# Optimization experiments

Measured on AMD Instinct MI355X. Metric: run time of the kernel, lower is better.

The kernel has to match this reference:

```python
import jax, jax.numpy as jnp
import numpy as np

CAL = {
 'x': (-0.0025095, 0.0022181),
 'onnxMatMul_166': (-0.22075387835502625, 0.208940327167511),
 'fc1MatMul': (-0.00291599917, 0.0017367251),
 'fc1bias': (-0.48688140511512756, 0.5176185369491577),
 'fc1Add': (-0.48778465390205383, 0.5181604027748108),
 'Wiz_1': (-0.43284985423088074, 0.46175122261047363),
 'Wir_1': (-0.34401071071624756, 0.29191476106643677),
 'Win_1': (-0.3236880302429199, 0.39607325196266174),
 'Whz_1': (-1.8417714834213257, 1.7173254489898682),
 'Whr_1': (-1.1574513912200928, 1.0300449132919312),
 'Whn_1': (-0.7756922245025635, 0.9530389308929443),
 'biz_1': (-0.5063393712043762, 0.36664387583732605),
 'bir_1': (-0.07920225709676743, 0.20611026883125305),
 'bin_1': (-0.5539973378181458, 0.17938342690467834),
 'bhz_1': (-0.5337516665458679, 0.4148772358894348),
 'bhr_1': (-0.07688436657190323, 0.14814253151416779),
 'bhn_1': (-0.7828555107116699, 0.9008108973503113),
 'Wiz_2': (-0.9102030992507935, 0.9408696889877319),
 'Wir_2': (-0.9560997486114502, 0.6683358550071716),
 'Win_2': (-0.4721935987472534, 0.48561596870422363),
 'Whz_2': (-1.2992678880691528, 1.2991048097610474),
 'Whr_2': (-0.8318714499473572, 1.1085889339447021),
 'Whn_2': (-0.955470085144043, 1.046797513961792),
 'biz_2': (-0.44805487990379333, 0.1560053527355194),
 'bir_2': (-0.08767592161893845, 0.11347303539514542),
 'bin_2': (-0.239909827709198, 0.12033259868621826),
 'bhz_2': (-0.43745461106300354, 0.12699371576309204),
 'bhr_2': (-0.09617264568805695, 0.07690174877643585),
 'bhn_2': (-0.17204178869724274, 0.19739042222499847),
 'onnxMatMul_207': (-1.3657219409942627, 1.158295750617981),
 'fc2bias': (-0.1750922054052353, 0.1385071724653244),
 'onnxMatMul_208': (-3.1666038036346436, 2.5026357173919678),
 'fc3bias': (-0.10188056528568268, 0.0899151861667633),
 'onnxMatMul_209': (-1.300571084022522, 1.928941249847412),
 'fc4bias': (-0.10699586570262909, 0.04597663879394531),
 'h1': (-0.002647488145157695, 0.0028339680284261703),
 'h2': (-0.0031016061548143625, 0.0030250486452132463),
 'gru1_a_': (-0.6389939785003662, 0.7715625762939453),
 'gru1_a': (-0.6046768426895142, 0.8871182203292847),
 'gru1_b_': (-0.004922409541904926, 0.004103424027562141),
 'gru1_b': (-0.07475128024816513, 0.14630259573459625),
 'gru1_c_': (-1.5660111904144287, 1.0454494953155518),
 'gru1_c': (-1.9779117107391357, 1.3700535297393799),
 'gru1_d_': (-0.008429044857621193, 0.006403823848813772),
 'gru1_d': (-0.5529640316963196, 0.41507571935653687),
 'gru1_e_': (-1.3637111186981201, 1.018247127532959),
 'gru1_e': (-1.8583884239196777, 1.1587692499160767),
 'gru1_f_': (-0.005411399528384209, 0.0061536869034171104),
 'gru1_f': (-0.7833794355392456, 0.8978855013847351),
 'gru1_r_': (-0.6226556301116943, 0.9800534844398499),
 'gru1_r': (0.3491777181625366, 0.7271188497543335),
 'gru1_z_': (-2.392332077026367, 1.7851293087005615),
 'gru1_z': (0.08375928550958633, 0.856329083442688),
 'gru1_n1': (-0.5516456365585327, 0.4556601643562317),
 'gru1_n2': (-2.4100341796875, 1.1423156261444092),
 'gru1_n': (-0.983996570110321, 0.8151924014091492),
 'gru1_hn1': (0.143670916557312, 0.9162406921386719),
 'gru1_hn2': (-0.9015777111053467, 0.45391541719436646),
 'gru1_hn3': (-0.0016954239690676332, 0.0016671211924403906),
 'rnn1GRU': (-0.9016271829605103, 0.4546271562576294),
 'gru2_a_': (-0.681461751461029, 0.9113116264343262),
 'gru2_a': (-0.7149235010147095, 0.908741295337677),
 'gru2_b_': (-0.005148397758603096, 0.011014967225492),
 'gru2_b': (-0.09436552226543427, 0.07623167335987091),
 'gru2_c_': (-1.2279887199401855, 1.1102137565612793),
 'gru2_c': (-1.6760436296463013, 1.200895071029663),
 'gru2_d_': (-0.008141756057739258, 0.00894666276872158),
 'gru2_d': (-0.43875735998153687, 0.1262134611606598),
 'gru2_e_': (-0.6732944250106812, 0.6314664483070374),
}
# calib entries for gru2 past 'e_' were truncated in the source; reuse gru1 ranges
for _k in ['e', 'f_', 'f', 'r_', 'r', 'z_', 'z', 'n1', 'n2', 'n', 'hn1', 'hn2', 'hn3']:
    CAL.setdefault('gru2_' + _k, CAL['gru1_' + _k])
CAL['rnn2GRU'] = CAL['rnn1GRU']


def fq(x, name):
    """Per-tensor unsigned 8-bit fake-quantize/dequantize (CalibrationParam S/Z)."""
    mn, mx = CAL[name]
    s = (mx - mn) / 255.0  # 2**8 - 1
    z = float(round(-mn / s))
    q = jnp.clip(jnp.round(x / s) + z, 0.0, 255.0)
    y = (q - z) * s
    # straight-through: forward value is exact fake-quant, identity gradient
    return x + jax.lax.stop_gradient(y - x)


def _gru_layer(xs, Wiz, Wir, Win, Whz, Whr, Whn, biz, bir, binn, bhz, bhr, bhn, L):
    p = 'gru%d' % L
    Wiz = fq(Wiz, 'Wiz_%d' % L); Wir = fq(Wir, 'Wir_%d' % L); Win = fq(Win, 'Win_%d' % L)
    Whz = fq(Whz, 'Whz_%d' % L); Whr = fq(Whr, 'Whr_%d' % L); Whn = fq(Whn, 'Whn_%d' % L)
    biz = fq(biz, 'biz_%d' % L); bir = fq(bir, 'bir_%d' % L); binn = fq(binn, 'bin_%d' % L)
    bhz = fq(bhz, 'bhz_%d' % L); bhr = fq(bhr, 'bhr_%d' % L); bhn = fq(bhn, 'bhn_%d' % L)
    # input projections batched over all timesteps (xs: [T,B,H] time-major)
    A = fq(fq(jnp.einsum('tbi,ih->tbh', xs, Wir), p + '_a_') + bir, p + '_a')
    C = fq(fq(jnp.einsum('tbi,ih->tbh', xs, Wiz), p + '_c_') + biz, p + '_c')
    E = fq(fq(jnp.einsum('tbi,ih->tbh', xs, Win), p + '_e_') + binn, p + '_e')
    h0 = fq(jnp.zeros((xs.shape[1], Whz.shape[0]), xs.dtype), 'h%d' % L)

    def step(h, ace):
        a, c, e = ace
        b = fq(fq(h @ Whr, p + '_b_') + bhr, p + '_b')
        r = fq(jax.nn.sigmoid(fq(a + b, p + '_r_')), p + '_r')
        d = fq(fq(h @ Whz, p + '_d_') + bhz, p + '_d')
        z = fq(jax.nn.sigmoid(fq(c + d, p + '_z_')), p + '_z')
        f = fq(fq(h @ Whn, p + '_f_') + bhn, p + '_f')
        n = fq(jnp.tanh(fq(e + fq(r * f, p + '_n1'), p + '_n2')), p + '_n')
        hn2 = fq(fq(1.0 - z, p + '_hn1') * n, p + '_hn2')
        hn3 = fq(z * h, p + '_hn3')
        h_new = fq(hn2 + hn3, 'rnn%dGRU' % L)
        return h_new, h_new

    _, hs = jax.lax.scan(step, h0, (A, C, E))
    return hs


def setup_inputs() -> dict:
    B, T, F, H, D = 64, 1000, 257, 400, 600
    ks = iter(jax.random.split(jax.random.key(0), 64))

    def u(shape, name):
        mn, mx = CAL[name]
        return jax.random.uniform(next(ks), shape, jnp.float32, mn, mx)

    inp = {}
    inp['x'] = jax.random.normal(next(ks), (B, T, F), jnp.float32) * 0.001
    inp['W_fc1'] = u((F, H), 'onnxMatMul_166')
    inp['b_fc1'] = u((H,), 'fc1bias')
    for L in (1, 2):
        for g in ('z', 'r', 'n'):
            inp['Wi%s%d' % (g, L)] = u((H, H), 'Wi%s_%d' % (g, L))
            inp['Wh%s%d' % (g, L)] = u((H, H), 'Wh%s_%d' % (g, L))
            inp['bi%s%d' % (g, L)] = u((H,), 'bi%s_%d' % (g, L))
            inp['bh%s%d' % (g, L)] = u((H,), 'bh%s_%d' % (g, L))
    inp['W_fc2'] = u((H, D), 'onnxMatMul_207'); inp['b_fc2'] = u((D,), 'fc2bias')
    inp['W_fc3'] = u((D, D), 'onnxMatMul_208'); inp['b_fc3'] = u((D,), 'fc3bias')
    inp['W_fc4'] = u((D, F), 'onnxMatMul_209'); inp['b_fc4'] = u((F,), 'fc4bias')
    return inp


def reference(x, W_fc1, b_fc1, Wiz1, Wir1, Win1, Whz1, Whr1, Whn1, biz1, bir1, bin1, bhz1, bhr1, bhn1, Wiz2, Wir2, Win2, Whz2, Whr2, Whn2, biz2, bir2, bin2, bhz2, bhr2, bhn2, W_fc2, b_fc2, W_fc3, b_fc3, W_fc4, b_fc4):
    xq = fq(x, 'x')
    t = fq(jnp.einsum('bti,ih->bth', xq, fq(W_fc1, 'onnxMatMul_166')), 'fc1MatMul')
    t = fq(t + fq(b_fc1, 'fc1bias'), 'fc1Add')
    xs = jnp.swapaxes(t, 0, 1)  # [T,B,400]
    h1 = _gru_layer(xs, Wiz1, Wir1, Win1, Whz1, Whr1, Whn1, biz1, bir1, bin1, bhz1, bhr1, bhn1, 1)
    h2 = _gru_layer(h1, Wiz2, Wir2, Win2, Whz2, Whr2, Whn2, biz2, bir2, bin2, bhz2, bhr2, bhn2, 2)
    y = jnp.swapaxes(h2, 0, 1)  # [B,T,400]
    y = jax.nn.relu(jnp.einsum('bth,hd->btd', y, fq(W_fc2, 'onnxMatMul_207')) + fq(b_fc2, 'fc2bias'))
    y = jax.nn.relu(jnp.einsum('btd,de->bte', y, fq(W_fc3, 'onnxMatMul_208')) + fq(b_fc3, 'fc3bias'))
    y = jax.nn.sigmoid(jnp.einsum('bte,ef->btf', y, fq(W_fc4, 'onnxMatMul_209')) + fq(b_fc4, 'fc4bias'))
    return y
```

## Files before the change

kernel.cpp:

```cpp
#include <hip/hip_runtime.h>
#include <math.h>

#define DEV static __device__ __forceinline__

typedef int v4i __attribute__((ext_vector_type(4)));
typedef float v4f __attribute__((ext_vector_type(4)));
typedef __bf16 bf16_t;
typedef __bf16 v8bf __attribute__((ext_vector_type(8)));

struct SZ { float s, z; };

constexpr double cfloor_(double v){ long long i=(long long)v; return ((double)i > v) ? (double)(i-1) : (double)i; }
constexpr double cround_(double v){
  double fl = cfloor_(v); double fr = v - fl;
  return (fr > 0.5) ? fl + 1.0 : (fr < 0.5 ? fl : ((((long long)fl) & 1LL) == 0 ? fl : fl + 1.0));
}
constexpr SZ mksz(double mn, double mx){
  double s = (mx - mn) / 255.0;
  double z = cround_(-mn / s);
  return SZ{ (float)s, (float)z };
}

constexpr SZ Zx     = mksz(-0.0025095, 0.0022181);
constexpr SZ ZW1    = mksz(-0.22075387835502625, 0.208940327167511);
// ... 42 lines not shown
constexpr SZ Ze1  = mksz(-1.8583884239196777, 1.1587692499160767);
constexpr SZ Zf_1 = mksz(-0.005411399528384209, 0.0061536869034171104);
constexpr SZ Zf1  = mksz(-0.7833794355392456, 0.8978855013847351);
constexpr SZ Zr_1 = mksz(-0.6226556301116943, 0.9800534844398499);
constexpr SZ Zr1  = mksz(0.3491777181625366, 0.7271188497543335);
constexpr SZ Zz_1 = mksz(-2.392332077026367, 1.7851293087005615);
constexpr SZ Zz1  = mksz(0.08375928550958633, 0.856329083442688);
constexpr SZ Zn11 = mksz(-0.5516456365585327, 0.4556601643562317);
constexpr SZ Zn21 = mksz(-2.4100341796875, 1.1423156261444092);
constexpr SZ Zn1  = mksz(-0.983996570110321, 0.8151924014091492);
constexpr SZ Zhn11= mksz(0.143670916557312, 0.9162406921386719);
constexpr SZ Zhn21= mksz(-0.9015777111053467, 0.45391541719436646);
constexpr SZ Zhn31= mksz(-0.0016954239690676332, 0.0016671211924403906);
constexpr SZ Zrnn = mksz(-0.9016271829605103, 0.4546271562576294);
constexpr SZ Za_2 = mksz(-0.681461751461029, 0.9113116264343262);
constexpr SZ Za2  = mksz(-0.7149235010147095, 0.908741295337677);
constexpr SZ Zb_2 = mksz(-0.005148397758603096, 0.011014967225492);
constexpr SZ Zb2g = mksz(-0.09436552226543427, 0.07623167335987091);
constexpr SZ Zc_2 = mksz(-1.2279887199401855, 1.1102137565612793);
constexpr SZ Zc2  = mksz(-1.6760436296463013, 1.200895071029663);
constexpr SZ Zd_2 = mksz(-0.008141756057739258, 0.00894666276872158);
constexpr SZ Zd2  = mksz(-0.43875735998153687, 0.1262134611606598);
constexpr SZ Ze_2 = mksz(-0.6732944250106812, 0.6314664483070374);

struct RecP {
  SZ wr, wz, wn;
  SZ a, c, e;
  SZ b1, b2, d1, d2, f1, f2;
  SZ r1, r2, z1, z2;
  SZ n1, n2, n3;
  SZ hn1, hn2, hn3, rnn;
};
constexpr RecP PL1 = { ZWhr1, ZWhz1, ZWhn1, Za1, Zc1, Ze1, Zb_1, Zb1, Zd_1, Zd1, Zf_1, Zf1,
                       Zr_1, Zr1, Zz_1, Zz1, Zn11, Zn21, Zn1, Zhn11, Zhn21, Zhn31, Zrnn };
constexpr RecP PL2 = { ZWhr2, ZWhz2, ZWhn2, Za2, Zc2, Ze1, Zb_2, Zb2g, Zd_2, Zd2, Zf_1, Zf1,
                       Zr_1, Zr1, Zz_1, Zz1, Zn11, Zn21, Zn1, Zhn11, Zhn21, Zhn31, Zrnn };

DEV float fq_(float x, float s, float z){
  float q = rintf(x / s) + z;
  q = fminf(fmaxf(q, 0.f), 255.f);
  return (q - z) * s;
}
DEV float sigm_(float v){ return 1.f / (1.f + expf(-v)); }

DEV unsigned udot4_(unsigned a, unsigned b, unsigned c){
#if defined(__has_builtin) && __has_builtin(__builtin_amdgcn_udot4)
  return __builtin_amdgcn_udot4(a, b, c, false);
#else
  return c + (a & 255u) * (b & 255u) + ((a >> 8) & 255u) * ((b >> 8) & 255u)
           + ((a >> 16) & 255u) * ((b >> 16) & 255u) + (a >> 24) * (b >> 24);
#endif
}

struct BJob { const float* src; float* dst; int n; float s; float z; };
struct BJobs { BJob j[16]; };
__global__ __launch_bounds__(256) void kbias(BJobs jobs){
  BJob J = jobs.j[blockIdx.x];
  for (int i = threadIdx.x; i < J.n; i += 256) J.dst[i] = fq_(J.src[i], J.s, J.z);
}

struct W6 { const float* W[6]; float s[6]; float z[6]; };
__global__ __launch_bounds__(256) void kwhc6(W6 jb, unsigned char* __restrict__ dst){
  int i = blockIdx.x * 256 + threadIdx.x;
  if (i < 960000) {
    int m = i / 160000, r = i - m * 160000;
    int j = r / 400, k = r - j * 400;
    float q = rintf(jb.W[m][k * 400 + j] / jb.s[m]) + jb.z[m];
    q = fminf(fmaxf(q, 0.f), 255.f);
    dst[i] = (unsigned char)q;
  }
}
__global__ __launch_bounds__(256) void kcolsum(const unsigned char* __restrict__ WhC, int* __restrict__ cs){
  int i = blockIdx.x * 256 + threadIdx.x;
  if (i < 2400) {
    const unsigned char* p = WhC + (size_t)i * 400;
    int s = 0;
    for (int k = 0; k < 400; ++k) s += p[k];
    cs[i] = s;
  }
}
__global__ __launch_bounds__(256) void kwic6(W6 jb, signed char* __restrict__ WiT, int* __restrict__ cs){
  for (int idx = blockIdx.x * 256 + threadIdx.x; idx < 960000; idx += gridDim.x * 256) {
    int m = idx / 160000, r = idx - m * 160000;
    int k = r / 400, n = r - k * 400;
    float q = rintf(jb.W[m][r] / jb.s[m]) + jb.z[m];
    q = fminf(fmaxf(q, 0.f), 255.f);
    int qi = (int)q;
    WiT[(size_t)m * 185600 + (size_t)n * 464 + k] = (signed char)(qi ^ 0x80);
    atomicAdd(&cs[m * 400 + n], qi - 128);
  }
  for (int idx = blockIdx.x * 256 + threadIdx.x; idx < 153600; idx += gridDim.x * 256) {
    int m = idx / 25600, r = idx - m * 25600;
    int n = r / 64, p = r - n * 64;
    WiT[(size_t)m * 185600 + (size_t)n * 464 + 400 + p] = 0;
  }
}
__global__ __launch_bounds__(256) void kwic(const float* __restrict__ W, signed char* __restrict__ Bt,
                                            int* __restrict__ cs, float s, float z, int K, int N){
  int total1 = K * N, total2 = (464 - K) * N;
  for (int idx = blockIdx.x * 256 + threadIdx.x; idx < total1; idx += gridDim.x * 256) {
    int k = idx / N, n = idx - k * N;
    float q = rintf(W[idx] / s) + z;
    q = fminf(fmaxf(q, 0.f), 255.f);
    int qi = (int)q;
    Bt[(size_t)n * 464 + k] = (signed char)(qi ^ 0x80);
    atomicAdd(&cs[n], qi - 128);
  }
  for (int idx = blockIdx.x * 256 + threadIdx.x; idx < total2; idx += gridDim.x * 256) {
    int n = idx / (464 - K), k = K + (idx - n * (464 - K));
    Bt[(size_t)n * 464 + k] = 0;
  }
}
__global__ __launch_bounds__(256) void kwbf(const float* __restrict__ W, bf16_t* __restrict__ Bt,
                                            float s, float z, int K, int N){
  int total1 = K * N, total2 = (608 - K) * N;
  for (int idx = blockIdx.x * 256 + threadIdx.x; idx < total1; idx += gridDim.x * 256) {
    int k = idx / N, n = idx - k * N;
    float q = rintf(W[idx] / s) + z;
    q = fminf(fmaxf(q, 0.f), 255.f);
    Bt[(size_t)n * 608 + k] = (bf16_t)(q - z);
  }
  for (int idx = blockIdx.x * 256 + threadIdx.x; idx < total2; idx += gridDim.x * 256) {
    int n = idx / (608 - K), k = K + (idx - n * (608 - K));
    Bt[(size_t)n * 608 + k] = (bf16_t)0.f;
  }
}
__global__ __launch_bounds__(256) void kxq(const float* __restrict__ x, unsigned char* __restrict__ xcq,
                                           float s, float z){
  int idx = blockIdx.x * 256 + threadIdx.x;
  if (idx < 64000 * 464) {
    int row = idx / 464, c = idx - row * 464;
    unsigned char code = 128;
    if (c < 257) {
      int bb = row & 63, tt = row >> 6;
      float q = rintf(x[((size_t)bb * 1000 + tt) * 257 + c] / s) + z;
      q = fminf(fmaxf(q, 0.f), 255.f);
      code = (unsigned char)q;
    }
    xcq[idx] = code;
  }
}
__global__ __launch_bounds__(256) void krsum(const unsigned char* __restrict__ A, int* __restrict__ rs,
                                             int w4){
  int r = blockIdx.x * 256 + threadIdx.x;
  const unsigned* p = (const unsigned*)(A + (size_t)r * (w4 * 16));
  unsigned s = 0;
  for (int i = 0; i < w4 * 4; ++i) s = udot4_(p[i], 0x01010101u, s);
  rs[r] = (int)s - 128 * 4 * (w4 * 4);
}
__global__ __launch_bounds__(256) void kinit2(unsigned long long* __restrict__ hp1,
                                              unsigned long long* __restrict__ hp2, unsigned code){
  int i = blockIdx.x * 256 + threadIdx.x;
  if (i < 25600) {
    unsigned long long w = (unsigned long long)(code * 0x01010101u);
    hp1[i] = w; hp2[i] = w;
  }
}

__global__ __launch_bounds__(256) void gemm_i8(
    const unsigned char* __restrict__ Au8, int strideA, int aw4,
    const int* __restrict__ rowsum,
    const signed char* __restrict__ Bt, const int* __restrict__ colsum,
    const float* __restrict__ bias,
    unsigned char* __restrict__ outU8, float* __restrict__ outF,
    int N, int nb, int outStride, int epMode,
    int czw, int cza, int cconst, float ss,
    float e1S, float e1Z, float e2S, float e2Z)
{
  __shared__ __align__(16) signed char Asl[64 * 464];
  __shared__ __align__(16) signed char Bsl[80 * 464];
  const int tid = threadIdx.x;
  const int bm = blockIdx.x / nb;
  const int bn = blockIdx.x - bm * nb;
  const int m0 = bm * 64;
  const int n0 = bn * 80;
  for (int i = tid; i < 80 * 29; i += 256) {
    int r = i / 29, c = i - r * 29;
    uint4 v;
    if (n0 + r < N) v = *(const uint4*)(Bt + (size_t)(n0 + r) * 464 + c * 16);
    else { v.x = 0u; v.y = 0u; v.z = 0u; v.w = 0u; }
    *(uint4*)(Bsl + (size_t)r * 464 + c * 16) = v;
  }
  for (int i = tid; i < 64 * 29; i += 256) {
    int r = i / 29, c = i - r * 29;
    uint4 v;
    if (c < aw4) {
      v = *(const uint4*)(Au8 + (size_t)(m0 + r) * strideA + c * 16);
      v.x ^= 0x80808080u; v.y ^= 0x80808080u; v.z ^= 0x80808080u; v.w ^= 0x80808080u;
    } else { v.x = 0u; v.y = 0u; v.z = 0u; v.w = 0u; }
    *(uint4*)(Asl + (size_t)r * 464 + c * 16) = v;
  }
  __syncthreads();
  const int wv = tid >> 6, ln = tid & 63;
  const int lr = ln & 15;
  const int lk = ln >> 4;
  v4i acc[5];
#pragma unroll
  for (int j = 0; j < 5; ++j) { acc[j][0] = 0; acc[j][1] = 0; acc[j][2] = 0; acc[j][3] = 0; }
#pragma unroll
  for (int kc = 0; kc < 7; ++kc) {
    int kb = kc * 64 + lk * 16;
    v4i a = *(const v4i*)(Asl + (size_t)(wv * 16 + lr) * 464 + kb);
#pragma unroll
    for (int j = 0; j < 5; ++j) {
      v4i b = *(const v4i*)(Bsl + (size_t)(j * 16 + lr) * 464 + kb);
      acc[j] = __builtin_amdgcn_mfma_i32_16x16x64_i8(a, b, acc[j], 0, 0, 0);
    }
  }
#pragma unroll
  for (int reg = 0; reg < 4; ++reg) {
    int row = m0 + wv * 16 + lk * 4 + reg;
    int RA = rowsum[row];
#pragma unroll
    for (int j = 0; j < 5; ++j) {
      int col = n0 + j * 16 + lr;
      if (col >= N) continue;
      int I = acc[j][reg] + czw * RA + cza * colsum[col] + cconst;
      float v = (float)I * ss;
      if (epMode == 0) {
        v = fq_(v, e1S, e1Z) + bias[col];
        float q = rintf(v / e2S) + e2Z;
        q = fminf(fmaxf(q, 0.f), 255.f);
        outU8[(size_t)row * outStride + col] = (unsigned char)q;
      } else {
        v += bias[col];
        v = fmaxf(v, 0.f);
        outF[(size_t)row * outStride + col] = v;
      }
    }
  }
}

__global__ __launch_bounds__(512) void gemm_bf(
    const float* __restrict__ A, const bf16_t* __restrict__ Bt,
    const float* __restrict__ bias, float* __restrict__ outF,
    int N, int nb, int epMode, int rowOff, float sc)
{
  __shared__ __align__(16) bf16_t Bs[128 * 616];
  const int tid = threadIdx.x;
  const int bm = blockIdx.x / nb;
  const int bn = blockIdx.x - bm * nb;
  const int m0 = bm * 128;
  const int n0 = bn * 128;
  for (int i = tid; i < 128 * 76; i += 512) {
    int r = i / 76, c = i - r * 76;
    uint4 v; v.x = 0u; v.y = 0u; v.z = 0u; v.w = 0u;
    if (n0 + r < N) v = *(const uint4*)((const char*)(Bt + (size_t)(n0 + r) * 608) + c * 16);
    *(uint4*)((char*)(Bs + (size_t)r * 616) + c * 16) = v;
  }
  __syncthreads();
  const int wv = tid >> 6, ln = tid & 63;
  const int lr = ln & 15, quad = ln >> 4;
  const float* arp = A + (size_t)(m0 + wv * 16 + lr) * 600;
  v4f acc[8];
#pragma unroll
  for (int j = 0; j < 8; ++j) { acc[j][0] = 0.f; acc[j][1] = 0.f; acc[j][2] = 0.f; acc[j][3] = 0.f; }
  for (int kc = 0; kc < 19; ++kc) {
    int kb = kc * 32 + quad * 8;
    float af[8];
    if (kc == 18 && quad == 3) {
#pragma unroll
      for (int j = 0; j < 8; ++j) af[j] = 0.f;
    } else {
      *(float4*)&af[0] = *(const float4*)(arp + kb);
      *(float4*)&af[4] = *(const float4*)(arp + kb + 4);
    }
    v8bf ah, al;
#pragma unroll
    for (int j = 0; j < 8; ++j) {
      float xx = af[j];
      bf16_t h = (bf16_t)xx;
      ah[j] = h;
      al[j] = (bf16_t)(xx - (float)h);
    }
#pragma unroll
    for (int nf = 0; nf < 8; ++nf) {
      v8bf bfrag = *(const v8bf*)(Bs + (size_t)(nf * 16 + lr) * 616 + kc * 32 + quad * 8);
      acc[nf] = __builtin_amdgcn_mfma_f32_16x16x32_bf16(ah, bfrag, acc[nf], 0, 0, 0);
      acc[nf] = __builtin_amdgcn_mfma_f32_16x16x32_bf16(al, bfrag, acc[nf], 0, 0, 0);
    }
  }
#pragma unroll
  for (int nf = 0; nf < 8; ++nf) {
    int col = n0 + nf * 16 + lr;
    if (col >= N) continue;
    float bcol = bias[col];
#pragma unroll
    for (int reg = 0; reg < 4; ++reg) {
      int row = m0 + wv * 16 + quad * 4 + reg;
      float v = acc[nf][reg] * sc + bcol;
      if (epMode == 2) {
        v = fmaxf(v, 0.f);
        outF[(size_t)row * N + col] = v;
      } else {
        v = sigm_(v);
        int rg = rowOff + row;
        int tt = rg >> 6, bb = rg & 63;
        outF[((size_t)bb * 1000 + tt) * 257 + col] = v;
      }
    }
  }
}

__global__ __launch_bounds__(512) void gru_rec4b(
    const unsigned char* __restrict__ WhC, const int* __restrict__ colsum,
    const unsigned char* __restrict__ Aq, const unsigned char* __restrict__ Cq,
    const unsigned char* __restrict__ Eq,
    const float* __restrict__ bhr, const float* __restrict__ bhz, const float* __restrict__ bhn,
    unsigned char* __restrict__ hs, unsigned long long* __restrict__ hpub, RecP P)
{
  __shared__ __align__(16) unsigned Wl[176 * 28];
  __shared__ __align__(16) unsigned hq[2][4 * 28];
  __shared__ int dots_i[300];
  __shared__ unsigned acew[2][75];
  __shared__ int ic_l[300];
  __shared__ float bias_l[300];
  __shared__ int HqS_s;

  const int tid = threadIdx.x;
  const int sl = blockIdx.x >> 6;
  const int b  = blockIdx.x & 63;
  const unsigned* Wu = (const unsigned*)WhC;

  unsigned wq[2][25];
#pragma unroll
  for (int s = 0; s < 2; ++s) {
    int q = tid + 512 * s;
    int ld = q >> 2, p = q & 3;
    int g = ld / 100, jl = ld - g * 100;
    int col = g * 400 + sl * 100 + jl;
    const unsigned* src = Wu + col * 100 + p * 25;
#pragma unroll
    for (int w = 0; w < 25; ++w) wq[s][w] = src[w];
  }
  if (tid < 176) {
    int q = 1024 + tid;
    int ld = q >> 2, p = q & 3;
    int g = ld / 100, jl = ld - g * 100;
    int col = g * 400 + sl * 100 + jl;
    const unsigned* src = Wu + col * 100 + p * 25;
    for (int w = 0; w < 25; ++w) Wl[tid * 28 + w] = src[w];
  }
  const int zh = (int)P.rnn.z;
  if (tid < 300) {
    int ld = tid;
    int g = ld / 100, jl = ld - g * 100;
    int col = g * 400 + sl * 100 + jl;
    int zw = (g == 0) ? (int)P.wr.z : (g == 1) ? (int)P.wz.z : (int)P.wn.z;
    ic_l[ld] = -zh * colsum[col] + 400 * zh * zw;
    bias_l[ld] = ((g == 0) ? bhr : (g == 1) ? bhz : bhn)[sl * 100 + jl];
  }
  const unsigned code0 = (unsigned)fminf(fmaxf(P.rnn.z, 0.f), 255.f);
  for (int i = tid; i < 100; i += 512)
    hq[0][(i / 25) * 28 + (i % 25)] = code0 * 0x01010101u;
  const unsigned char* psrc = nullptr;
  int poff = 0;
  if (tid < 75) {
    int g = tid / 25, w = tid - g * 25;
    psrc = (g == 0) ? Aq : (g == 1) ? Cq : Eq;
    poff = (sl * 25 + w) * 4;
    acew[0][tid] = *(const unsigned*)(psrc + (size_t)b * 400 + poff);
  }
  __syncthreads();

  const int part = tid & 3;
  const int grp = tid >> 2;
  const int zwr = (int)P.wr.z, zwz = (int)P.wz.z, zwn = (int)P.wn.z;
  const float swr = P.wr.s * P.rnn.s, swz = P.wz.s * P.rnn.s, swn = P.wn.s * P.rnn.s;

  unsigned hcode = code0;
  unsigned pf = 0;

  for (int t = 0; t < 1000; ++t) {
    if (tid < 75) {
      int tn = (t + 1 < 1000) ? (t + 1) : 999;
      pf = *(const unsigned*)(psrc + ((size_t)tn * 64 + b) * 400 + poff);
    }
    if (tid >= 448) {
      int lane = tid - 448;
      const unsigned long long* base = hpub + ((size_t)(t & 3) * 64 + b) * 100;
      unsigned pay0, pay1 = 0;
      {
        int o = lane / 25, p = lane - o * 25;
        int so = (sl + o + 1) & 3;
        const unsigned long long* src = base + so * 25 + p;
        unsigned long long w64;
        while ((unsigned)((w64 = __hip_atomic_load(src, __ATOMIC_RELAXED, __HIP_MEMORY_SCOPE_AGENT)) >> 32)
               != (unsigned)t) { }
        pay0 = (unsigned)w64;
        hq[t & 1][so * 28 + p] = pay0;
      }
      if (lane < 11) {
        int w1 = 64 + lane;
        int o = w1 / 25, p = w1 - o * 25;
        int so = (sl + o + 1) & 3;
        const unsigned long long* src = base + so * 25 + p;
        unsigned long long w64;
        while ((unsigned)((w64 = __hip_atomic_load(src, __ATOMIC_RELAXED, __HIP_MEMORY_SCOPE_AGENT)) >> 32)
               != (unsigned)t) { }
        pay1 = (unsigned)w64;
        hq[t & 1][so * 28 + p] = pay1;
      }
      unsigned ssum = udot4_(pay0, 0x01010101u, 0u);
      if (lane < 11) ssum = udot4_(pay1, 0x01010101u, ssum);
      if (lane < 25) ssum = udot4_(hq[t & 1][sl * 28 + lane], 0x01010101u, ssum);
#pragma unroll
      for (int off = 32; off; off >>= 1) ssum += __shfl_down(ssum, off, 64);
      if (lane == 0) HqS_s = (int)ssum;
    }
    __syncthreads();
    const unsigned* hb = &hq[t & 1][part * 28];
    const unsigned* wl = &Wl[tid * 28];
    unsigned a0 = 0, a1 = 0, a2 = 0;
#pragma unroll
    for (int c = 0; c < 6; ++c) {
      uint4 h4 = *(const uint4*)(hb + 4 * c);
      a0 = udot4_(wq[0][4*c+0], h4.x, a0);
      a0 = udot4_(wq[0][4*c+1], h4.y, a0);
      a0 = udot4_(wq[0][4*c+2], h4.z, a0);
      a0 = udot4_(wq[0][4*c+3], h4.w, a0);
      a1 = udot4_(wq[1][4*c+0], h4.x, a1);
      a1 = udot4_(wq[1][4*c+1], h4.y, a1);
      a1 = udot4_(wq[1][4*c+2], h4.z, a1);
      a1 = udot4_(wq[1][4*c+3], h4.w, a1);
      if (tid < 176) {
        uint4 w4 = *(const uint4*)(wl + 4 * c);
        a2 = udot4_(w4.x, h4.x, a2);
        a2 = udot4_(w4.y, h4.y, a2);
        a2 = udot4_(w4.z, h4.z, a2);
        a2 = udot4_(w4.w, h4.w, a2);
      }
    }
    {
      unsigned hl = hb[24];
      a0 = udot4_(wq[0][24], hl, a0);
      a1 = udot4_(wq[1][24], hl, a1);
      if (tid < 176) a2 = udot4_(wl[24], hl, a2);
    }
    a0 += __shfl_xor(a0, 1); a0 += __shfl_xor(a0, 2);
    a1 += __shfl_xor(a1, 1); a1 += __shfl_xor(a1, 2);
    a2 += __shfl_xor(a2, 1); a2 += __shfl_xor(a2, 2);
    if (part == 0)      dots_i[grp]       = (int)a0;
    else if (part == 1) dots_i[128 + grp] = (int)a1;
    else if (part == 2) { if (grp < 44) dots_i[256 + grp] = (int)a2; }
    __syncthreads();

    if (tid < 75) acew[(t + 1) & 1][tid] = pf;
    if (tid < 100) {
      const int j = tid;
      const unsigned char* ab = (const unsigned char*)&acew[t & 1][0];
      float av = ((float)ab[j]       - P.a.z) * P.a.s;
      float cv = ((float)ab[100 + j] - P.c.z) * P.c.s;
      float ev = ((float)ab[200 + j] - P.e.z) * P.e.s;
      int hqs = HqS_s;
      int Ib = dots_i[j]       - zwr * hqs + ic_l[j];
      int Id = dots_i[100 + j] - zwz * hqs + ic_l[100 + j];
      int If = dots_i[200 + j] - zwn * hqs + ic_l[200 + j];
      float bb = fq_((float)Ib * swr, P.b1.s, P.b1.z) + bias_l[j];
      bb = fq_(bb, P.b2.s, P.b2.z);
      float dd = fq_((float)Id * swz, P.d1.s, P.d1.z) + bias_l[100 + j];
      dd = fq_(dd, P.d2.s, P.d2.z);
      float ff = fq_((float)If * swn, P.f1.s, P.f1.z) + bias_l[200 + j];
      ff = fq_(ff, P.f2.s, P.f2.z);
      float r  = fq_(sigm_(fq_(av + bb, P.r1.s, P.r1.z)), P.r2.s, P.r2.z);
      float zz = fq_(sigm_(fq_(cv + dd, P.z1.s, P.z1.z)), P.z2.s, P.z2.z);
      float nn = fq_(tanhf(fq_(ev + fq_(r * ff, P.n1.s, P.n1.z), P.n2.s, P.n2.z)), P.n3.s, P.n3.z);
      float hold = ((float)hcode - P.rnn.z) * P.rnn.s;
      float hn2v = fq_(fq_(1.f - zz, P.hn1.s, P.hn1.z) * nn, P.hn2.s, P.hn2.z);
      float hn3v = fq_(zz * hold, P.hn3.s, P.hn3.z);
      float hnew = hn2v + hn3v;
      float qv = rintf(hnew / P.rnn.s) + P.rnn.z;
      qv = fminf(fmaxf(qv, 0.f), 255.f);
      unsigned code = (unsigned)qv;
      hcode = code;
      unsigned c1 = __shfl_down(code, 1);
      unsigned c2 = __shfl_down(code, 2);
      unsigned c3 = __shfl_down(code, 3);
      if ((j & 3) == 0) {
        unsigned packed = code | (c1 << 8) | (c2 << 16) | (c3 << 24);
        int wrd = j >> 2;
        hq[(t + 1) & 1][sl * 28 + wrd] = packed;
        *(unsigned*)(hs + ((size_t)t * 64 + b) * 400 + ((sl * 25 + wrd) << 2)) = packed;
        unsigned long long out64 = ((unsigned long long)(unsigned)(t + 1) << 32) | packed;
        unsigned long long* dst = hpub + ((size_t)((t + 1) & 3) * 64 + b) * 100 + sl * 25 + wrd;
        __hip_atomic_store(dst, out64, __ATOMIC_RELAXED, __HIP_MEMORY_SCOPE_AGENT);
      }
    }
    __syncthreads();
  }
}

extern "C" void kernel_launch(void* const* d_in, const int* in_sizes, int n_in,
                              void* d_out, int out_size, void* d_ws, size_t ws_size,
                              hipStream_t stream)
{
  const float* x    = (const float*)d_in[0];
  const float* Wfc1 = (const float*)d_in[1];
  const float* bfc1 = (const float*)d_in[2];
  const float* Wiz1 = (const float*)d_in[3];  const float* Whz1 = (const float*)d_in[4];
  const float* biz1 = (const float*)d_in[5];  const float* bhz1 = (const float*)d_in[6];
  const float* Wir1 = (const float*)d_in[7];  const float* Whr1 = (const float*)d_in[8];
  const float* bir1 = (const float*)d_in[9];  const float* bhr1 = (const float*)d_in[10];
  const float* Win1 = (const float*)d_in[11]; const float* Whn1 = (const float*)d_in[12];
  const float* bin1 = (const float*)d_in[13]; const float* bhn1 = (const float*)d_in[14];
  const float* Wiz2 = (const float*)d_in[15]; const float* Whz2 = (const float*)d_in[16];
  const float* biz2 = (const float*)d_in[17]; const float* bhz2 = (const float*)d_in[18];
  const float* Wir2 = (const float*)d_in[19]; const float* Whr2 = (const float*)d_in[20];
  const float* bir2 = (const float*)d_in[21]; const float* bhr2 = (const float*)d_in[22];
  const float* Win2 = (const float*)d_in[23]; const float* Whn2 = (const float*)d_in[24];
  const float* bin2 = (const float*)d_in[25]; const float* bhn2 = (const float*)d_in[26];
  const float* Wfc2 = (const float*)d_in[27]; const float* bfc2 = (const float*)d_in[28];
  const float* Wfc3 = (const float*)d_in[29]; const float* bfc3 = (const float*)d_in[30];
  const float* Wfc4 = (const float*)d_in[31]; const float* bfc4 = (const float*)d_in[32];
  float* out = (float*)d_out;

  char* wp = (char*)d_ws;
  auto alloc = [&](size_t bytes) -> void* {
    void* p = (void*)wp;
    wp += (bytes + 255) & ~(size_t)255;
    return p;
  };
  float* b1q = (float*)alloc(400 * 4);
  float* biq = (float*)alloc(2400 * 4);
  float* bhq = (float*)alloc(2400 * 4);
  float* b2q = (float*)alloc(600 * 4);
  float* b3q = (float*)alloc(600 * 4);
  float* b4q = (float*)alloc(257 * 4);
  unsigned char* WhC = (unsigned char*)alloc(960000);
  int* colsum = (int*)alloc(2400 * 4);
  signed char* WiT = (signed char*)alloc(7 * 400 * 464);
  signed char* Bt2 = (signed char*)alloc(600 * 464);
  bf16_t* Bt3 = (bf16_t*)alloc(600 * 608 * 2);
  bf16_t* Bt4 = (bf16_t*)alloc(257 * 608 * 2);
  int* cwi = (int*)alloc((7 * 400 + 600) * 4);
  int* rsX1 = (int*)alloc(64000 * 4);
  int* rsX  = (int*)alloc(64000 * 4);
  int* rsH  = (int*)alloc(64000 * 4);
  int* rsH2 = (int*)alloc(64000 * 4);
  unsigned char* xsq = (unsigned char*)alloc(25600000);
  unsigned char* Aq  = (unsigned char*)alloc(25600000);
  unsigned char* Cq  = (unsigned char*)alloc(25600000);
  unsigned char* Eq  = (unsigned char*)alloc(25600000);
  unsigned char* hs1 = (unsigned char*)alloc(25600000);
  unsigned char* hs2 = (unsigned char*)alloc(25600000);
  unsigned long long* hpub1 = (unsigned long long*)alloc(25600 * 8);
  unsigned long long* hpub2 = (unsigned long long*)alloc(25600 * 8);
  float* y2c = (float*)Aq;
  float* y3c = (float*)(Aq + 38400000);
  unsigned char* xcq = hs1;

  BJobs bj;
  bj.j[0]  = { bfc1, b1q,        400, Zbfc1.s, Zbfc1.z };
  bj.j[1]  = { bir1, biq + 0,    400, Zbir1.s, Zbir1.z };
  bj.j[2]  = { biz1, biq + 400,  400, Zbiz1.s, Zbiz1.z };
  bj.j[3]  = { bin1, biq + 800,  400, Zbin1.s, Zbin1.z };
  bj.j[4]  = { bir2, biq + 1200, 400, Zbir2.s, Zbir2.z };
  bj.j[5]  = { biz2, biq + 1600, 400, Zbiz2.s, Zbiz2.z };
  bj.j[6]  = { bin2, biq + 2000, 400, Zbin2.s, Zbin2.z };
  bj.j[7]  = { bhr1, bhq + 0,    400, Zbhr1.s, Zbhr1.z };
  bj.j[8]  = { bhz1, bhq + 400,  400, Zbhz1.s, Zbhz1.z };
  bj.j[9]  = { bhn1, bhq + 800,  400, Zbhn1.s, Zbhn1.z };
  bj.j[10] = { bhr2, bhq + 1200, 400, Zbhr2.s, Zbhr2.z };
  bj.j[11] = { bhz2, bhq + 1600, 400, Zbhz2.s, Zbhz2.z };
  bj.j[12] = { bhn2, bhq + 2000, 400, Zbhn2.s, Zbhn2.z };
  bj.j[13] = { bfc2, b2q,        600, Zbfc2.s, Zbfc2.z };
  bj.j[14] = { bfc3, b3q,        600, Zbfc3.s, Zbfc3.z };
  bj.j[15] = { bfc4, b4q,        257, Zbfc4.s, Zbfc4.z };
  kbias<<<dim3(16), dim3(256), 0, stream>>>(bj);

  W6 wh = { { Whr1, Whz1, Whn1, Whr2, Whz2, Whn2 },
            { ZWhr1.s, ZWhz1.s, ZWhn1.s, ZWhr2.s, ZWhz2.s, ZWhn2.s },
            { ZWhr1.z, ZWhz1.z, ZWhn1.z, ZWhr2.z, ZWhz2.z, ZWhn2.z } };
  kwhc6<<<dim3(3750), dim3(256), 0, stream>>>(wh, WhC);
  kcolsum<<<dim3(10), dim3(256), 0, stream>>>(WhC, colsum);
  unsigned code0 = (unsigned)(Zrnn.z < 0.f ? 0.f : (Zrnn.z > 255.f ? 255.f : Zrnn.z));
  kinit2<<<dim3(100), dim3(256), 0, stream>>>(hpub1, hpub2, code0);

  hipMemsetAsync(cwi, 0, (7 * 400 + 600) * 4, stream);
  W6 wi = { { Wir1, Wiz1, Win1, Wir2, Wiz2, Win2 },
            { ZWir1.s, ZWiz1.s, ZWin1.s, ZWir2.s, ZWiz2.s, ZWin2.s },
            { ZWir1.z, ZWiz1.z, ZWin1.z, ZWir2.z, ZWiz2.z, ZWin2.z } };
  kwic6<<<dim3(625), dim3(256), 0, stream>>>(wi, WiT, cwi);
  kwic<<<dim3(625), dim3(256), 0, stream>>>(Wfc1, WiT + (size_t)6 * 185600, cwi + 2400, ZW1.s, ZW1.z, 257, 400);
  kwic<<<dim3(625), dim3(256), 0, stream>>>(Wfc2, Bt2, cwi + 2800, ZWfc2.s, ZWfc2.z, 400, 600);
  kwbf<<<dim3(625), dim3(256), 0, stream>>>(Wfc3, Bt3, ZWfc3.s, ZWfc3.z, 600, 600);
  kwbf<<<dim3(625), dim3(256), 0, stream>>>(Wfc4, Bt4, ZWfc4.s, ZWfc4.z, 600, 257);

  auto gi8 = [&](const unsigned char* A, int strideA, int aw4, const int* rs,
                 const signed char* Bt, const int* cs, const float* bias,
                 unsigned char* oU8, float* oF, int M, int N, int outStride, int epMode,
                 SZ a, SZ w, int Kreal, float ss, SZ e1, SZ e2) {
    int czw = 128 - (int)w.z, cza = 128 - (int)a.z;
    int cconst = Kreal * cza * czw;
    int nb = (N + 79) / 80;
    gemm_i8<<<dim3((M / 64) * nb), dim3(256), 0, stream>>>(
        A, strideA, aw4, rs, Bt, cs, bias, oU8, oF, N, nb, outStride, epMode,
        czw, cza, cconst, ss, e1.s, e1.z, e2.s, e2.z);
  };

  kxq<<<dim3((64000 * 464 + 255) / 256), dim3(256), 0, stream>>>(x, xcq, Zx.s, Zx.z);
  krsum<<<dim3(250), dim3(256), 0, stream>>>(xcq, rsX1, 29);
  gi8(xcq, 464, 29, rsX1, WiT + (size_t)6 * 185600, cwi + 2400, b1q,
      xsq, nullptr, 64000, 400, 400, 0, Zx, ZW1, 257, Zx.s * ZW1.s, Zfc1mm, Zfc1add);

  krsum<<<dim3(250), dim3(256), 0, stream>>>(xsq, rsX, 25);
  gi8(xsq, 400, 25, rsX, WiT + (size_t)0 * 185600, cwi + 0,    biq + 0,   Aq, nullptr,
      64000, 400, 400, 0, Zfc1add, ZWir1, 400, Zfc1add.s * ZWir1.s, Za_1, Za1);
  gi8(xsq, 400, 25, rsX, WiT + (size_t)1 * 185600, cwi + 400,  biq + 400, Cq, nullptr,
      64000, 400, 400, 0, Zfc1add, ZWiz1, 400, Zfc1add.s * ZWiz1.s, Zc_1, Zc1);
  gi8(xsq, 400, 25, rsX, WiT + (size_t)2 * 185600, cwi + 800,  biq + 800, Eq, nullptr,
      64000, 400, 400, 0, Zfc1add, ZWin1, 400, Zfc1add.s * ZWin1.s, Ze_1, Ze1);
  gru_rec4b<<<dim3(256), dim3(512), 0, stream>>>(WhC, colsum, Aq, Cq, Eq,
                                                 bhq + 0, bhq + 400, bhq + 800,
                                                 hs1, hpub1, PL1);
  krsum<<<dim3(250), dim3(256), 0, stream>>>(hs1, rsH, 25);
  gi8(hs1, 400, 25, rsH, WiT + (size_t)3 * 185600, cwi + 1200, biq + 1200, Aq, nullptr,
      64000, 400, 400, 0, Zrnn, ZWir2, 400, Zrnn.s * ZWir2.s, Za_2, Za2);
  gi8(hs1, 400, 25, rsH, WiT + (size_t)4 * 185600, cwi + 1600, biq + 1600, Cq, nullptr,
      64000, 400, 400, 0, Zrnn, ZWiz2, 400, Zrnn.s * ZWiz2.s, Zc_2, Zc2);
  gi8(hs1, 400, 25, rsH, WiT + (size_t)5 * 185600, cwi + 2000, biq + 2000, Eq, nullptr,
      64000, 400, 400, 0, Zrnn, ZWin2, 400, Zrnn.s * ZWin2.s, Ze_2, Ze1);
  gru_rec4b<<<dim3(256), dim3(512), 0, stream>>>(WhC + 480000, colsum + 1200, Aq, Cq, Eq,
                                                 bhq + 1200, bhq + 1600, bhq + 2000,
                                                 hs2, hpub2, PL2);
  krsum<<<dim3(250), dim3(256), 0, stream>>>(hs2, rsH2, 25);
  for (int rc = 0; rc < 4; ++rc) {
    const unsigned char* a2 = hs2 + (size_t)rc * 16000 * 400;
    gi8(a2, 400, 25, rsH2 + rc * 16000, Bt2, cwi + 2800, b2q, nullptr, y2c,
        16000, 600, 600, 2, Zrnn, ZWfc2, 400, Zrnn.s * ZWfc2.s, Zrnn, Zrnn);
    gemm_bf<<<dim3(125 * 5), dim3(512), 0, stream>>>(y2c, Bt3, b3q, y3c, 600, 5, 2, 0, ZWfc3.s);
    gemm_bf<<<dim3(125 * 3), dim3(512), 0, stream>>>(y3c, Bt4, b4q, out, 257, 3, 3, rc * 16000, ZWfc4.s);
  }
  (void)in_sizes; (void)n_in; (void)out_size; (void)ws_size;
}
```

Measured before the change: 7.138 ms.

## Process two batch rows per GRU recurrence block with interleaved phases

The persistent GRU recurrence kernel now handles two batch elements (b and b+32) per workgroup, halving the grid from 256 to 128 blocks. Each time step runs the two rows back to back, so one row's cross-block wait for the hidden state can overlap with the other row's compute. An LDS flag with acquire/release spin-waits replaces the first barrier, letting compute waves start once the poller has filled the hidden vector. This doubles the serial work per block per step and adds intra-block spinning, in exchange for fewer blocks contending on the global handoff.

```diff
diff --git a/kernel.cpp b/kernel.cpp
--- a/kernel.cpp
+++ b/kernel.cpp
@@ -368,7 +368,7 @@
   }
 }
 
-__global__ __launch_bounds__(512) void gru_rec4b(
+__global__ __launch_bounds__(512) void gru_rec4b2(
     const unsigned char* __restrict__ WhC, const int* __restrict__ colsum,
     const unsigned char* __restrict__ Aq, const unsigned char* __restrict__ Cq,
     const unsigned char* __restrict__ Eq,
@@ -376,16 +376,18 @@
     unsigned char* __restrict__ hs, unsigned long long* __restrict__ hpub, RecP P)
 {
   __shared__ __align__(16) unsigned Wl[176 * 28];
-  __shared__ __align__(16) unsigned hq[2][4 * 28];
-  __shared__ int dots_i[300];
-  __shared__ unsigned acew[2][75];
+  __shared__ __align__(16) unsigned hq[2][2][4 * 28];
+  __shared__ int dots_i[2][300];
+  __shared__ unsigned acew[2][2][75];
   __shared__ int ic_l[300];
   __shared__ float bias_l[300];
-  __shared__ int HqS_s;
+  __shared__ int HqS_s[2];
+  __shared__ int flag[2];
 
   const int tid = threadIdx.x;
-  const int sl = blockIdx.x >> 6;
-  const int b  = blockIdx.x & 63;
+  const int sl = blockIdx.x >> 5;
+  const int bA = blockIdx.x & 31;
+  const int bB = bA + 32;
   const unsigned* Wu = (const unsigned*)WhC;
 
   unsigned wq[2][25];
@@ -417,15 +419,20 @@
     bias_l[ld] = ((g == 0) ? bhr : (g == 1) ? bhz : bhn)[sl * 100 + jl];
   }
   const unsigned code0 = (unsigned)fminf(fmaxf(P.rnn.z, 0.f), 255.f);
-  for (int i = tid; i < 100; i += 512)
-    hq[0][(i / 25) * 28 + (i % 25)] = code0 * 0x01010101u;
+  for (int i = tid; i < 100; i += 512) {
+    int idx = (i / 25) * 28 + (i % 25);
+    hq[0][0][idx] = code0 * 0x01010101u;
+    hq[1][0][idx] = code0 * 0x01010101u;
+  }
+  if (tid == 0) { flag[0] = -1; flag[1] = -1; }
   const unsigned char* psrc = nullptr;
   int poff = 0;
   if (tid < 75) {
     int g = tid / 25, w = tid - g * 25;
     psrc = (g == 0) ? Aq : (g == 1) ? Cq : Eq;
     poff = (sl * 25 + w) * 4;
-    acew[0][tid] = *(const unsigned*)(psrc + (size_t)b * 400 + poff);
+    acew[0][0][tid] = *(const unsigned*)(psrc + (size_t)bA * 400 + poff);
+    acew[1][0][tid] = *(const unsigned*)(psrc + (size_t)bB * 400 + poff);
   }
   __syncthreads();
 
@@ -434,17 +441,19 @@
   const int zwr = (int)P.wr.z, zwz = (int)P.wz.z, zwn = (int)P.wn.z;
   const float swr = P.wr.s * P.rnn.s, swz = P.wz.s * P.rnn.s, swn = P.wn.s * P.rnn.s;
 
-  unsigned hcode = code0;
-  unsigned pf = 0;
+  unsigned hcodeA = code0, hcodeB = code0;
+  unsigned pfA = 0, pfB = 0;
 
   for (int t = 0; t < 1000; ++t) {
     if (tid < 75) {
       int tn = (t + 1 < 1000) ? (t + 1) : 999;
-      pf = *(const unsigned*)(psrc + ((size_t)tn * 64 + b) * 400 + poff);
-    }
+      pfA = *(const unsigned*)(psrc + ((size_t)tn * 64 + bA) * 400 + poff);
+      pfB = *(const unsigned*)(psrc + ((size_t)tn * 64 + bB) * 400 + poff);
+    }
+
     if (tid >= 448) {
       int lane = tid - 448;
-      const unsigned long long* base = hpub + ((size_t)(t & 3) * 64 + b) * 100;
+      const unsigned long long* base = hpub + ((size_t)(t & 3) * 64 + bA) * 100;
       unsigned pay0, pay1 = 0;
       {
         int o = lane / 25, p = lane - o * 25;
@@ -454,7 +463,7 @@
         while ((unsigned)((w64 = __hip_atomic_load(src, __ATOMIC_RELAXED, __HIP_MEMORY_SCOPE_AGENT)) >> 32)
                != (unsigned)t) { }
         pay0 = (unsigned)w64;
-        hq[t & 1][so * 28 + p] = pay0;
+        hq[0][t & 1][so * 28 + p] = pay0;
       }
       if (lane < 11) {
         int w1 = 64 + lane;
@@ -465,63 +474,67 @@
         while ((unsigned)((w64 = __hip_atomic_load(src, __ATOMIC_RELAXED, __HIP_MEMORY_SCOPE_AGENT)) >> 32)
                != (unsigned)t) { }
         pay1 = (unsigned)w64;
-        hq[t & 1][so * 28 + p] = pay1;
-      }
+        hq[0][t & 1][so * 28 + p] = pay1;
+      }
+      if (lane == 0)
+        __hip_atomic_store(&flag[0], t, __ATOMIC_RELEASE, __HIP_MEMORY_SCOPE_WORKGROUP);
       unsigned ssum = udot4_(pay0, 0x01010101u, 0u);
       if (lane < 11) ssum = udot4_(pay1, 0x01010101u, ssum);
-      if (lane < 25) ssum = udot4_(hq[t & 1][sl * 28 + lane], 0x01010101u, ssum);
+      if (lane < 25) ssum = udot4_(hq[0][t & 1][sl * 28 + lane], 0x01010101u, ssum);
 #pragma unroll
       for (int off = 32; off; off >>= 1) ssum += __shfl_down(ssum, off, 64);
-      if (lane == 0) HqS_s = (int)ssum;
+      if (lane == 0) HqS_s[0] = (int)ssum;
+    } else {
+      while (__hip_atomic_load(&flag[0], __ATOMIC_ACQUIRE, __HIP_MEMORY_SCOPE_WORKGROUP) < t) { }
+    }
+    {
+      const unsigned* hb = &hq[0][t & 1][part * 28];
+      const unsigned* wl = &Wl[tid * 28];
+      unsigned a0 = 0, a1 = 0, a2 = 0;
+#pragma unroll
+      for (int c = 0; c < 6; ++c) {
+        uint4 h4 = *(const uint4*)(hb + 4 * c);
+        a0 = udot4_(wq[0][4*c+0], h4.x, a0);
+        a0 = udot4_(wq[0][4*c+1], h4.y, a0);
+        a0 = udot4_(wq[0][4*c+2], h4.z, a0);
+        a0 = udot4_(wq[0][4*c+3], h4.w, a0);
+        a1 = udot4_(wq[1][4*c+0], h4.x, a1);
+        a1 = udot4_(wq[1][4*c+1], h4.y, a1);
+        a1 = udot4_(wq[1][4*c+2], h4.z, a1);
+        a1 = udot4_(wq[1][4*c+3], h4.w, a1);
+        if (tid < 176) {
+          uint4 w4 = *(const uint4*)(wl + 4 * c);
+          a2 = udot4_(w4.x, h4.x, a2);
+          a2 = udot4_(w4.y, h4.y, a2);
+          a2 = udot4_(w4.z, h4.z, a2);
+          a2 = udot4_(w4.w, h4.w, a2);
+        }
+      }
+      {
+        unsigned hl = hb[24];
+        a0 = udot4_(wq[0][24], hl, a0);
+        a1 = udot4_(wq[1][24], hl, a1);
+        if (tid < 176) a2 = udot4_(wl[24], hl, a2);
+      }
+      a0 += __shfl_xor(a0, 1); a0 += __shfl_xor(a0, 2);
+      a1 += __shfl_xor(a1, 1); a1 += __shfl_xor(a1, 2);
+      a2 += __shfl_xor(a2, 1); a2 += __shfl_xor(a2, 2);
+      if (part == 0)      dots_i[0][grp]       = (int)a0;
+      else if (part == 1) dots_i[0][128 + grp] = (int)a1;
+      else if (part == 2) { if (grp < 44) dots_i[0][256 + grp] = (int)a2; }
     }
     __syncthreads();
-    const unsigned* hb = &hq[t & 1][part * 28];
-    const unsigned* wl = &Wl[tid * 28];
-    unsigned a0 = 0, a1 = 0, a2 = 0;
-#pragma unroll
-    for (int c = 0; c < 6; ++c) {
-      uint4 h4 = *(const uint4*)(hb + 4 * c);
-      a0 = udot4_(wq[0][4*c+0], h4.x, a0);
-      a0 = udot4_(wq[0][4*c+1], h4.y, a0);
-      a0 = udot4_(wq[0][4*c+2], h4.z, a0);
-      a0 = udot4_(wq[0][4*c+3], h4.w, a0);
-      a1 = udot4_(wq[1][4*c+0], h4.x, a1);
-      a1 = udot4_(wq[1][4*c+1], h4.y, a1);
-      a1 = udot4_(wq[1][4*c+2], h4.z, a1);
-      a1 = udot4_(wq[1][4*c+3], h4.w, a1);
-      if (tid < 176) {
-        uint4 w4 = *(const uint4*)(wl + 4 * c);
-        a2 = udot4_(w4.x, h4.x, a2);
-        a2 = udot4_(w4.y, h4.y, a2);
-        a2 = udot4_(w4.z, h4.z, a2);
-        a2 = udot4_(w4.w, h4.w, a2);
-      }
-    }
-    {
-      unsigned hl = hb[24];
-      a0 = udot4_(wq[0][24], hl, a0);
-      a1 = udot4_(wq[1][24], hl, a1);
-      if (tid < 176) a2 = udot4_(wl[24], hl, a2);
-    }
-    a0 += __shfl_xor(a0, 1); a0 += __shfl_xor(a0, 2);
-    a1 += __shfl_xor(a1, 1); a1 += __shfl_xor(a1, 2);
-    a2 += __shfl_xor(a2, 1); a2 += __shfl_xor(a2, 2);
-    if (part == 0)      dots_i[grp]       = (int)a0;
-    else if (part == 1) dots_i[128 + grp] = (int)a1;
-    else if (part == 2) { if (grp < 44) dots_i[256 + grp] = (int)a2; }
-    __syncthreads();
-
-    if (tid < 75) acew[(t + 1) & 1][tid] = pf;
+    if (tid < 75) acew[0][(t + 1) & 1][tid] = pfA;
     if (tid < 100) {
       const int j = tid;
-      const unsigned char* ab = (const unsigned char*)&acew[t & 1][0];
+      const unsigned char* ab = (const unsigned char*)&acew[0][t & 1][0];
       float av = ((float)ab[j]       - P.a.z) * P.a.s;
       float cv = ((float)ab[100 + j] - P.c.z) * P.c.s;
       float ev = ((float)ab[200 + j] - P.e.z) * P.e.s;
-      int hqs = HqS_s;
-      int Ib = dots_i[j]       - zwr * hqs + ic_l[j];
-      int Id = dots_i[100 + j] - zwz * hqs + ic_l[100 + j];
-      int If = dots_i[200 + j] - zwn * hqs + ic_l[200 + j];
+      int hqs = HqS_s[0];
+      int Ib = dots_i[0][j]       - zwr * hqs + ic_l[j];
+      int Id = dots_i[0][100 + j] - zwz * hqs + ic_l[100 + j];
+      int If = dots_i[0][200 + j] - zwn * hqs + ic_l[200 + j];
       float bb = fq_((float)Ib * swr, P.b1.s, P.b1.z) + bias_l[j];
       bb = fq_(bb, P.b2.s, P.b2.z);
       float dd = fq_((float)Id * swz, P.d1.s, P.d1.z) + bias_l[100 + j];
@@ -531,24 +544,140 @@
       float r  = fq_(sigm_(fq_(av + bb, P.r1.s, P.r1.z)), P.r2.s, P.r2.z);
       float zz = fq_(sigm_(fq_(cv + dd, P.z1.s, P.z1.z)), P.z2.s, P.z2.z);
       float nn = fq_(tanhf(fq_(ev + fq_(r * ff, P.n1.s, P.n1.z), P.n2.s, P.n2.z)), P.n3.s, P.n3.z);
-      float hold = ((float)hcode - P.rnn.z) * P.rnn.s;
+      float hold = ((float)hcodeA - P.rnn.z) * P.rnn.s;
       float hn2v = fq_(fq_(1.f - zz, P.hn1.s, P.hn1.z) * nn, P.hn2.s, P.hn2.z);
       float hn3v = fq_(zz * hold, P.hn3.s, P.hn3.z);
       float hnew = hn2v + hn3v;
       float qv = rintf(hnew / P.rnn.s) + P.rnn.z;
       qv = fminf(fmaxf(qv, 0.f), 255.f);
       unsigned code = (unsigned)qv;
-      hcode = code;
+      hcodeA = code;
       unsigned c1 = __shfl_down(code, 1);
       unsigned c2 = __shfl_down(code, 2);
       unsigned c3 = __shfl_down(code, 3);
       if ((j & 3) == 0) {
         unsigned packed = code | (c1 << 8) | (c2 << 16) | (c3 << 24);
         int wrd = j >> 2;
-        hq[(t + 1) & 1][sl * 28 + wrd] = packed;
-        *(unsigned*)(hs + ((size_t)t * 64 + b) * 400 + ((sl * 25 + wrd) << 2)) = packed;
+        hq[0][(t + 1) & 1][sl * 28 + wrd] = packed;
+        *(unsigned*)(hs + ((size_t)t * 64 + bA) * 400 + ((sl * 25 + wrd) << 2)) = packed;
         unsigned long long out64 = ((unsigned long long)(unsigned)(t + 1) << 32) | packed;
-        unsigned long long* dst = hpub + ((size_t)((t + 1) & 3) * 64 + b) * 100 + sl * 25 + wrd;
+        unsigned long long* dst = hpub + ((size_t)((t + 1) & 3) * 64 + bA) * 100 + sl * 25 + wrd;
+        __hip_atomic_store(dst, out64, __ATOMIC_RELAXED, __HIP_MEMORY_SCOPE_AGENT);
+      }
+    }
+    __syncthreads();
+
+    if (tid >= 448) {
+      int lane = tid - 448;
+      const unsigned long long* base = hpub + ((size_t)(t & 3) * 64 + bB) * 100;
+      unsigned pay0, pay1 = 0;
+      {
+        int o = lane / 25, p = lane - o * 25;
+        int so = (sl + o + 1) & 3;
+        const unsigned long long* src = base + so * 25 + p;
+        unsigned long long w64;
+        while ((unsigned)((w64 = __hip_atomic_load(src, __ATOMIC_RELAXED, __HIP_MEMORY_SCOPE_AGENT)) >> 32)
+               != (unsigned)t) { }
+        pay0 = (unsigned)w64;
+        hq[1][t & 1][so * 28 + p] = pay0;
+      }
+      if (lane < 11) {
+        int w1 = 64 + lane;
+        int o = w1 / 25, p = w1 - o * 25;
+        int so = (sl + o + 1) & 3;
+        const unsigned long long* src = base + so * 25 + p;
+        unsigned long long w64;
+        while ((unsigned)((w64 = __hip_atomic_load(src, __ATOMIC_RELAXED, __HIP_MEMORY_SCOPE_AGENT)) >> 32)
+               != (unsigned)t) { }
+        pay1 = (unsigned)w64;
+        hq[1][t & 1][so * 28 + p] = pay1;
+      }
+      if (lane == 0)
+        __hip_atomic_store(&flag[1], t, __ATOMIC_RELEASE, __HIP_MEMORY_SCOPE_WORKGROUP);
+      unsigned ssum = udot4_(pay0, 0x01010101u, 0u);
+      if (lane < 11) ssum = udot4_(pay1, 0x01010101u, ssum);
+      if (lane < 25) ssum = udot4_(hq[1][t & 1][sl * 28 + lane], 0x01010101u, ssum);
+#pragma unroll
+      for (int off = 32; off; off >>= 1) ssum += __shfl_down(ssum, off, 64);
+      if (lane == 0) HqS_s[1] = (int)ssum;
+    } else {
+      while (__hip_atomic_load(&flag[1], __ATOMIC_ACQUIRE, __HIP_MEMORY_SCOPE_WORKGROUP) < t) { }
+    }
+    {
+      const unsigned* hb = &hq[1][t & 1][part * 28];
+      const unsigned* wl = &Wl[tid * 28];
+      unsigned a0 = 0, a1 = 0, a2 = 0;
+#pragma unroll
+      for (int c = 0; c < 6; ++c) {
+        uint4 h4 = *(const uint4*)(hb + 4 * c);
+        a0 = udot4_(wq[0][4*c+0], h4.x, a0);
+        a0 = udot4_(wq[0][4*c+1], h4.y, a0);
+        a0 = udot4_(wq[0][4*c+2], h4.z, a0);
+        a0 = udot4_(wq[0][4*c+3], h4.w, a0);
+        a1 = udot4_(wq[1][4*c+0], h4.x, a1);
+        a1 = udot4_(wq[1][4*c+1], h4.y, a1);
+        a1 = udot4_(wq[1][4*c+2], h4.z, a1);
+        a1 = udot4_(wq[1][4*c+3], h4.w, a1);
+        if (tid < 176) {
+          uint4 w4 = *(const uint4*)(wl + 4 * c);
+          a2 = udot4_(w4.x, h4.x, a2);
+          a2 = udot4_(w4.y, h4.y, a2);
+          a2 = udot4_(w4.z, h4.z, a2);
+          a2 = udot4_(w4.w, h4.w, a2);
+        }
+      }
+      {
+        unsigned hl = hb[24];
+        a0 = udot4_(wq[0][24], hl, a0);
+        a1 = udot4_(wq[1][24], hl, a1);
+        if (tid < 176) a2 = udot4_(wl[24], hl, a2);
+      }
+      a0 += __shfl_xor(a0, 1); a0 += __shfl_xor(a0, 2);
+      a1 += __shfl_xor(a1, 1); a1 += __shfl_xor(a1, 2);
+      a2 += __shfl_xor(a2, 1); a2 += __shfl_xor(a2, 2);
+      if (part == 0)      dots_i[1][grp]       = (int)a0;
+      else if (part == 1) dots_i[1][128 + grp] = (int)a1;
+      else if (part == 2) { if (grp < 44) dots_i[1][256 + grp] = (int)a2; }
+    }
+    __syncthreads();
+    if (tid < 75) acew[1][(t + 1) & 1][tid] = pfB;
+    if (tid < 100) {
+      const int j = tid;
+      const unsigned char* ab = (const unsigned char*)&acew[1][t & 1][0];
+      float av = ((float)ab[j]       - P.a.z) * P.a.s;
+      float cv = ((float)ab[100 + j] - P.c.z) * P.c.s;
+      float ev = ((float)ab[200 + j] - P.e.z) * P.e.s;
+      int hqs = HqS_s[1];
+      int Ib = dots_i[1][j]       - zwr * hqs + ic_l[j];
+      int Id = dots_i[1][100 + j] - zwz * hqs + ic_l[100 + j];
+      int If = dots_i[1][200 + j] - zwn * hqs + ic_l[200 + j];
+      float bb = fq_((float)Ib * swr, P.b1.s, P.b1.z) + bias_l[j];
+      bb = fq_(bb, P.b2.s, P.b2.z);
+      float dd = fq_((float)Id * swz, P.d1.s, P.d1.z) + bias_l[100 + j];
+      dd = fq_(dd, P.d2.s, P.d2.z);
+      float ff = fq_((float)If * swn, P.f1.s, P.f1.z) + bias_l[200 + j];
+      ff = fq_(ff, P.f2.s, P.f2.z);
+      float r  = fq_(sigm_(fq_(av + bb, P.r1.s, P.r1.z)), P.r2.s, P.r2.z);
+      float zz = fq_(sigm_(fq_(cv + dd, P.z1.s, P.z1.z)), P.z2.s, P.z2.z);
+      float nn = fq_(tanhf(fq_(ev + fq_(r * ff, P.n1.s, P.n1.z), P.n2.s, P.n2.z)), P.n3.s, P.n3.z);
+      float hold = ((float)hcodeB - P.rnn.z) * P.rnn.s;
+      float hn2v = fq_(fq_(1.f - zz, P.hn1.s, P.hn1.z) * nn, P.hn2.s, P.hn2.z);
+      float hn3v = fq_(zz * hold, P.hn3.s, P.hn3.z);
+      float hnew = hn2v + hn3v;
+      float qv = rintf(hnew / P.rnn.s) + P.rnn.z;
+      qv = fminf(fmaxf(qv, 0.f), 255.f);
+      unsigned code = (unsigned)qv;
+      hcodeB = code;
+      unsigned c1 = __shfl_down(code, 1);
+      unsigned c2 = __shfl_down(code, 2);
+      unsigned c3 = __shfl_down(code, 3);
+      if ((j & 3) == 0) {
+        unsigned packed = code | (c1 << 8) | (c2 << 16) | (c3 << 24);
+        int wrd = j >> 2;
+        hq[1][(t + 1) & 1][sl * 28 + wrd] = packed;
+        *(unsigned*)(hs + ((size_t)t * 64 + bB) * 400 + ((sl * 25 + wrd) << 2)) = packed;
+        unsigned long long out64 = ((unsigned long long)(unsigned)(t + 1) << 32) | packed;
+        unsigned long long* dst = hpub + ((size_t)((t + 1) & 3) * 64 + bB) * 100 + sl * 25 + wrd;
         __hip_atomic_store(dst, out64, __ATOMIC_RELAXED, __HIP_MEMORY_SCOPE_AGENT);
       }
     }
@@ -676,9 +805,9 @@
       64000, 400, 400, 0, Zfc1add, ZWiz1, 400, Zfc1add.s * ZWiz1.s, Zc_1, Zc1);
   gi8(xsq, 400, 25, rsX, WiT + (size_t)2 * 185600, cwi + 800,  biq + 800, Eq, nullptr,
       64000, 400, 400, 0, Zfc1add, ZWin1, 400, Zfc1add.s * ZWin1.s, Ze_1, Ze1);
-  gru_rec4b<<<dim3(256), dim3(512), 0, stream>>>(WhC, colsum, Aq, Cq, Eq,
-                                                 bhq + 0, bhq + 400, bhq + 800,
-                                                 hs1, hpub1, PL1);
+  gru_rec4b2<<<dim3(128), dim3(512), 0, stream>>>(WhC, colsum, Aq, Cq, Eq,
+                                                  bhq + 0, bhq + 400, bhq + 800,
+                                                  hs1, hpub1, PL1);
   krsum<<<dim3(250), dim3(256), 0, stream>>>(hs1, rsH, 25);
   gi8(hs1, 400, 25, rsH, WiT + (size_t)3 * 185600, cwi + 1200, biq + 1200, Aq, nullptr,
       64000, 400, 400, 0, Zrnn, ZWir2, 400, Zrnn.s * ZWir2.s, Za_2, Za2);
@@ -686,9 +815,9 @@
       64000, 400, 400, 0, Zrnn, ZWiz2, 400, Zrnn.s * ZWiz2.s, Zc_2, Zc2);
   gi8(hs1, 400, 25, rsH, WiT + (size_t)5 * 185600, cwi + 2000, biq + 2000, Eq, nullptr,
       64000, 400, 400, 0, Zrnn, ZWin2, 400, Zrnn.s * ZWin2.s, Ze_2, Ze1);
-  gru_rec4b<<<dim3(256), dim3(512), 0, stream>>>(WhC + 480000, colsum + 1200, Aq, Cq, Eq,
-                                                 bhq + 1200, bhq + 1600, bhq + 2000,
-                                                 hs2, hpub2, PL2);
+  gru_rec4b2<<<dim3(128), dim3(512), 0, stream>>>(WhC + 480000, colsum + 1200, Aq, Cq, Eq,
+                                                  bhq + 1200, bhq + 1600, bhq + 2000,
+                                                  hs2, hpub2, PL2);
   krsum<<<dim3(250), dim3(256), 0, stream>>>(hs2, rsH2, 25);
   for (int rc = 0; rc < 4; ++rc) {
     const unsigned char* a2 = hs2 + (size_t)rc * 16000 * 400;
```

Result: slower. 11.00 ms (+54.1%).
